# Kernel optimization log

Measured on AMD Instinct MI355X. Metric: run time of the kernel, lower is better.

The kernel has to match this reference:

```python
import jax, jax.numpy as jnp
import numpy as np

S, B, E = 2048, 8, 1024  # seq_len, batch, embed_dim
GAMMA = 0.5              # Kernel(gamma=0.5)


def setup_inputs() -> dict:
    key = jax.random.key(0)
    ks = jax.random.split(key, 4)
    # Weight scale 1/E keeps pairwise squared distances O(1) so the RBF
    # kernel weights are well-conditioned (exp doesn't underflow to all-zeros).
    w_scale = 1.0 / E
    inputs = jax.random.normal(ks[0], (S, B, E), dtype=jnp.float32)
    Wq = jax.random.normal(ks[1], (E, E), dtype=jnp.float32) * w_scale
    Wk = jax.random.normal(ks[2], (E, E), dtype=jnp.float32) * w_scale
    Wv = jax.random.normal(ks[3], (E, E), dtype=jnp.float32) * w_scale
    bq = jnp.zeros((E,), jnp.float32)
    bk = jnp.zeros((E,), jnp.float32)
    bv = jnp.zeros((E,), jnp.float32)
    return {"inputs": inputs, "Wq": Wq, "bq": bq, "Wk": Wk, "bk": bk,
            "Wv": Wv, "bv": bv}


def reference(inputs, Wq, bq, Wk, bk, Wv, bv):
    # QKV projections (nn.Linear: x @ W.T + b)
    q = inputs @ Wq.T + bq  # (S, B, E)
    k = inputs @ Wk.T + bk  # (S, B, E)
    v = inputs @ Wv.T + bv  # (S, B, E)

    # Pairwise RBF kernel sim[t, j, b] = exp(-gamma * ||q[t,b] - k[j,b]||^2)
    # (vectorized replacement of the original O(S^2) python double loop),
    # via ||q||^2 + ||k||^2 - 2 q.k expansion (GEMM-shaped contraction).
    q2 = jnp.sum(q * q, axis=-1)                 # (S, B)
    k2 = jnp.sum(k * k, axis=-1)                 # (S, B)
    qk = jnp.einsum('tbe,jbe->tjb', q, k)        # (S, S, B)
    d2 = q2[:, None, :] + k2[None, :, :] - 2.0 * qk
    d2 = jnp.maximum(d2, 0.0)

    # sim / sim.sum(dim=1) with sim = exp(-gamma*d2) is exactly
    # softmax(-gamma*d2) over axis 1 (the j axis) -- numerically stable form.
    sim = jax.nn.softmax(-GAMMA * d2, axis=1)    # (S, S, B): (t, j, b)

    # Aggregate values: out[t, b, e] = sum_j sim[t, j, b] * v[j, b, e]
    return jnp.einsum('tjb,jbe->tbe', sim, v)    # (S, B, E)
```

## Files before the change

kernel.cpp:

```cpp
#include <hip/hip_runtime.h>
#include <stdint.h>

#define S_LEN 2048
#define BATCH 8
#define EMB   1024
#define GAMMA 0.5f

typedef unsigned short ushort_t;
typedef __attribute__((ext_vector_type(8))) short  short8;
typedef __attribute__((ext_vector_type(8))) unsigned short ushort8;
typedef __attribute__((ext_vector_type(4))) float  floatx4;

__device__ __forceinline__ ushort_t f2bf(float f) {
  uint32_t x = __float_as_uint(f);
  x += 0x7fffu + ((x >> 16) & 1u);
  return (ushort_t)(x >> 16);
}

__device__ __forceinline__ void gl_lds16(const ushort_t* g, ushort_t* l) {
  __builtin_amdgcn_global_load_lds(
      (const __attribute__((address_space(1))) unsigned int*)g,
      (__attribute__((address_space(3))) unsigned int*)l, 16, 0, 0);
}


__device__ __forceinline__ void stage_half(const ushort_t* __restrict__ G,
                                           int ld, int kcol,
                                           ushort_t* lregion, int wave, int lane) {
  const int r4 = lane >> 2;
  const int slot = (lane & 3) ^ ((r4 >> 1) & 3);
  const ushort_t* g = G + (size_t)(wave * 32 + r4) * ld + kcol + slot * 8;
  gl_lds16(g, lregion + wave * 1024);
  gl_lds16(g + (size_t)16 * ld, lregion + wave * 1024 + 512);
}

__device__ __forceinline__ short8 lds_frag(const ushort_t* region, int row, int q) {
  return *(const short8*)(region + row * 32 + (((q ^ (row >> 1)) & 3) << 3));
}

#define MFMA_16(AR, B0, B1, J0, J1)                                            \
  __builtin_amdgcn_s_setprio(1);                                               \
  _Pragma("unroll")                                                            \
  for (int i = 0; i < 8; ++i) {                                                \
    acc[i][J0] = __builtin_amdgcn_mfma_f32_16x16x32_bf16(AR[i], B0, acc[i][J0], 0, 0, 0); \
    acc[i][J1] = __builtin_amdgcn_mfma_f32_16x16x32_bf16(AR[i], B1, acc[i][J1], 0, 0, 0); \
  }                                                                            \
  __builtin_amdgcn_s_setprio(0);

#define INTERVAL_OPEN()                                                        \
  __builtin_amdgcn_s_barrier();                                                \
  asm volatile("s_waitcnt lgkmcnt(0)" ::: "memory");                           \
  __builtin_amdgcn_sched_barrier(0);

__device__ __forceinline__ void gemm8_core(
    const ushort_t* __restrict__ A, const ushort_t* __restrict__ B,
    int lda, int ldb, int K, ushort_t* smem, floatx4 (&acc)[8][4])
{
  const int tid = threadIdx.x;
  const int wave = tid >> 6, lane = tid & 63;
  const int wm = wave >> 2, wn = wave & 3;
  const int lr = lane & 15, q = lane >> 4;
  const int NT = K >> 6;
  const int ra = wm * 128 + lr;
  const int rb = wn * 64 + lr;

  stage_half(A, lda, 0,  smem +     0, wave, lane);
  stage_half(B, ldb, 0,  smem + 16384, wave, lane);
  stage_half(A, lda, 32, smem +  8192, wave, lane);
  stage_half(B, ldb, 32, smem + 24576, wave, lane);
  stage_half(A, lda, 64, smem + 32768, wave, lane);
  stage_half(B, ldb, 64, smem + 49152, wave, lane);
  stage_half(A, lda, 96, smem + 40960, wave, lane);
  asm volatile("s_waitcnt vmcnt(6)" ::: "memory");
  __builtin_amdgcn_s_barrier();
  __builtin_amdgcn_sched_barrier(0);

  short8 ar[8], ar2[8], b0, b1, t0, t1, u0, u1;
#pragma unroll
  for (int i = 0; i < 8; ++i) ar[i] = lds_frag(smem, ra + i * 16, q);
  b0 = lds_frag(smem + 16384, rb,      q);
  b1 = lds_frag(smem + 16384, rb + 16, q);

  for (int kt = 0; kt < NT; ++kt) {
    ushort_t* const cur = smem + (kt & 1) * 32768;
    ushort_t* const nxt = smem + ((kt & 1) ^ 1) * 32768;
    const bool s1 = (kt + 1) < NT, s2 = (kt + 2) < NT;

    INTERVAL_OPEN()
    MFMA_16(ar, b0, b1, 0, 1)
    t0 = lds_frag(cur + 16384, rb + 32, q);
    t1 = lds_frag(cur + 16384, rb + 48, q);
#pragma unroll
    for (int i = 0; i < 4; ++i) ar2[i] = lds_frag(cur + 8192, ra + i * 16, q);
    if (s1) stage_half(B, ldb, (kt + 1) * 64 + 32, nxt + 24576, wave, lane);

    INTERVAL_OPEN()
    MFMA_16(ar, t0, t1, 2, 3)
#pragma unroll
    for (int i = 4; i < 8; ++i) ar2[i] = lds_frag(cur + 8192, ra + i * 16, q);
    u0 = lds_frag(cur + 24576, rb,      q);
    u1 = lds_frag(cur + 24576, rb + 16, q);
    if (s2) stage_half(A, lda, (kt + 2) * 64, cur, wave, lane);

    INTERVAL_OPEN()
    MFMA_16(ar2, u0, u1, 0, 1)
    t0 = lds_frag(cur + 24576, rb + 32, q);
    t1 = lds_frag(cur + 24576, rb + 48, q);
    if (s2) stage_half(B, ldb, (kt + 2) * 64, cur + 16384, wave, lane);
    if (s1) {
      if (s2) { asm volatile("s_waitcnt vmcnt(4)" ::: "memory"); }
      else    { asm volatile("s_waitcnt vmcnt(0)" ::: "memory"); }
    }

    INTERVAL_OPEN()
    MFMA_16(ar2, t0, t1, 2, 3)
    if (s1) {
#pragma unroll
      for (int i = 0; i < 8; ++i) ar[i] = lds_frag(nxt, ra + i * 16, q);
      b0 = lds_frag(nxt + 16384, rb,      q);
      b1 = lds_frag(nxt + 16384, rb + 16, q);
    }
    if (s2) stage_half(A, lda, (kt + 2) * 64 + 32, cur + 8192, wave, lane);
  }
}

__global__ __launch_bounds__(256) void k_quant_x(const float* __restrict__ X,
                                                 ushort_t* __restrict__ Xb) {
  size_t i = ((size_t)blockIdx.x * 256 + threadIdx.x) * 4;
  float4 v = *(const float4*)(X + i);
  *(ushort4*)(Xb + i) = make_ushort4(f2bf(v.x), f2bf(v.y), f2bf(v.z), f2bf(v.w));
}

__global__ __launch_bounds__(256) void k_quant_w(
    const float* __restrict__ Wq, const float* __restrict__ Wk,
    const float* __restrict__ Wv, ushort_t* __restrict__ W) {
  size_t i = ((size_t)blockIdx.x * 256 + threadIdx.x) * 4;
  int row = (int)(i >> 10), col = (int)(i & 1023);
  int sel = row >> 10, sr = row & 1023;
  const float* src = sel == 0 ? Wq : (sel == 1 ? Wk : Wv);
  float4 v = *(const float4*)(src + (size_t)sr * 1024 + col);
  *(ushort4*)(W + i) = make_ushort4(f2bf(v.x), f2bf(v.y), f2bf(v.z), f2bf(v.w));
}

__global__ __launch_bounds__(256) void k_bias_zero(
    const float* __restrict__ bq, const float* __restrict__ bk,
    const float* __restrict__ bv, float* __restrict__ bias,
    float* __restrict__ q2, float* __restrict__ k2, float* __restrict__ rsum) {
  int i = blockIdx.x * 256 + threadIdx.x;
  if (i < 1024)       bias[i] = bq[i];
  else if (i < 2048)  bias[i] = bk[i - 1024];
  else if (i < 3072)  bias[i] = bv[i - 2048];
  if (i < BATCH * S_LEN) { q2[i] = 0.f; k2[i] = 0.f; rsum[i] = 0.f; }
}

__global__ __launch_bounds__(512, 2) void k_gemm_qkv(
    const ushort_t* __restrict__ Xb, const ushort_t* __restrict__ W,
    const float* __restrict__ bias,
    ushort_t* __restrict__ Q, ushort_t* __restrict__ Kp, ushort_t* __restrict__ V,
    float* __restrict__ q2, float* __restrict__ k2) {
  __shared__ __attribute__((aligned(16))) ushort_t smem[65536];
  const int mt = blockIdx.x * 256, nt = blockIdx.y * 256;
  floatx4 acc[8][4];
  const floatx4 z = {0.f, 0.f, 0.f, 0.f};
#pragma unroll
  for (int i = 0; i < 8; ++i)
#pragma unroll
    for (int j = 0; j < 4; ++j) acc[i][j] = z;

  gemm8_core(Xb + (size_t)mt * EMB, W + (size_t)nt * EMB, EMB, EMB, EMB, smem, acc);

  const int lane = threadIdx.x & 63, wave = threadIdx.x >> 6;
  const int wm = wave >> 2, wn = wave & 3;
  const int lr = lane & 15, q = lane >> 4;
  const int which = nt >> 10;
  const int nc0 = nt & 1023;
  ushort_t* dst = which == 0 ? Q : (which == 1 ? Kp : V);
  float* sq = which == 0 ? q2 : k2;
  float bv4[4];
#pragma unroll
  for (int j = 0; j < 4; ++j) bv4[j] = bias[nt + wn * 64 + j * 16 + lr];

#pragma unroll
  for (int i = 0; i < 8; ++i) {
#pragma unroll
    for (int r = 0; r < 4; ++r) {
      const int g = mt + wm * 128 + i * 16 + q * 4 + r;
      const int t = g >> 3, b = g & 7;
      float ss = 0.f;
#pragma unroll
      for (int j = 0; j < 4; ++j) {
        const float val = acc[i][j][r] + bv4[j];
        dst[(size_t)(b * S_LEN + t) * EMB + nc0 + wn * 64 + j * 16 + lr] = f2bf(val);
        ss += val * val;
      }
      if (which < 2) {
        ss += __shfl_xor(ss, 1);
        ss += __shfl_xor(ss, 2);
        ss += __shfl_xor(ss, 4);
        ss += __shfl_xor(ss, 8);
        if (lr == 0) atomicAdd(&sq[b * S_LEN + t], ss);
      }
    }
  }
}

__global__ __launch_bounds__(256) void k_transpose(const ushort_t* __restrict__ V,
                                                   ushort_t* __restrict__ Vt) {
  __shared__ ushort_t tile[64][72];
  const int b = blockIdx.z, j0 = blockIdx.x * 64, e0 = blockIdx.y * 64;
  const ushort_t* src = V + ((size_t)b * S_LEN + j0) * EMB + e0;
  const int tid = threadIdx.x;
#pragma unroll
  for (int rep = 0; rep < 2; ++rep) {
    const int lin = rep * 256 + tid;
    const int j = lin >> 3, e8 = (lin & 7) * 8;
    *(uint4*)&tile[j][e8] = *(const uint4*)(src + (size_t)j * EMB + e8);
  }
  __syncthreads();
  ushort_t* dst = Vt + ((size_t)b * EMB + e0) * S_LEN + j0;
#pragma unroll
  for (int rep = 0; rep < 2; ++rep) {
    const int lin = rep * 256 + tid;
    const int e = lin >> 3, j8 = (lin & 7) * 8;
    ushort8 o;
#pragma unroll
    for (int m = 0; m < 8; ++m) o[m] = tile[j8 + m][e];
    *(ushort8*)(dst + (size_t)e * S_LEN + j8) = o;
  }
}

__global__ __launch_bounds__(512, 2) void k_logits(
    const ushort_t* __restrict__ Q, const ushort_t* __restrict__ Kp,
    const float* __restrict__ q2, const float* __restrict__ k2,
    ushort_t* __restrict__ P, float* __restrict__ rsum) {
  __shared__ __attribute__((aligned(16))) ushort_t smem[65536];
  const int b = blockIdx.z;
  const int mt = blockIdx.x * 256, nt = blockIdx.y * 256;
  floatx4 acc[8][4];
  const floatx4 z = {0.f, 0.f, 0.f, 0.f};
#pragma unroll
  for (int i = 0; i < 8; ++i)
#pragma unroll
    for (int j = 0; j < 4; ++j) acc[i][j] = z;

  gemm8_core(Q + ((size_t)b * S_LEN + mt) * EMB,
             Kp + ((size_t)b * S_LEN + nt) * EMB, EMB, EMB, EMB, smem, acc);

  const int lane = threadIdx.x & 63, wave = threadIdx.x >> 6;
  const int wm = wave >> 2, wn = wave & 3;
  const int lr = lane & 15, q = lane >> 4;
  float k2v[4];
#pragma unroll
  for (int j = 0; j < 4; ++j) k2v[j] = k2[b * S_LEN + nt + wn * 64 + j * 16 + lr];

#pragma unroll
  for (int i = 0; i < 8; ++i) {
#pragma unroll
    for (int r = 0; r < 4; ++r) {
      const int t = mt + wm * 128 + i * 16 + q * 4 + r;
      const float q2v = q2[b * S_LEN + t];
      float ss = 0.f;
#pragma unroll
      for (int j = 0; j < 4; ++j) {
        float d2 = q2v + k2v[j] - 2.f * acc[i][j][r];
        d2 = fmaxf(d2, 0.f);
        const float p = __expf(-GAMMA * d2);
        P[((size_t)b * S_LEN + t) * S_LEN + nt + wn * 64 + j * 16 + lr] = f2bf(p);
        ss += p;
      }
      ss += __shfl_xor(ss, 1);
      ss += __shfl_xor(ss, 2);
      ss += __shfl_xor(ss, 4);
      ss += __shfl_xor(ss, 8);
      if (lr == 0) atomicAdd(&rsum[b * S_LEN + t], ss);
    }
  }
}

__global__ __launch_bounds__(512, 2) void k_out(
    const ushort_t* __restrict__ P, const ushort_t* __restrict__ Vt,
    const float* __restrict__ rsum, float* __restrict__ out) {
  __shared__ __attribute__((aligned(16))) ushort_t smem[65536];
  const int b = blockIdx.z;
  const int mt = blockIdx.x * 256, nt = blockIdx.y * 256;
  floatx4 acc[8][4];
  const floatx4 z = {0.f, 0.f, 0.f, 0.f};
#pragma unroll
  for (int i = 0; i < 8; ++i)
#pragma unroll
    for (int j = 0; j < 4; ++j) acc[i][j] = z;

  gemm8_core(P + ((size_t)b * S_LEN + mt) * S_LEN,
             Vt + ((size_t)b * EMB + nt) * S_LEN, S_LEN, S_LEN, S_LEN, smem, acc);

  const int lane = threadIdx.x & 63, wave = threadIdx.x >> 6;
  const int wm = wave >> 2, wn = wave & 3;
  const int lr = lane & 15, q = lane >> 4;
#pragma unroll
  for (int i = 0; i < 8; ++i) {
#pragma unroll
    for (int r = 0; r < 4; ++r) {
      const int t = mt + wm * 128 + i * 16 + q * 4 + r;
      const float rinv = 1.f / rsum[b * S_LEN + t];
#pragma unroll
      for (int j = 0; j < 4; ++j) {
        const int e = nt + wn * 64 + j * 16 + lr;
        out[((size_t)t * BATCH + b) * EMB + e] = acc[i][j][r] * rinv;
      }
    }
  }
}

extern "C" void kernel_launch(void* const* d_in, const int* in_sizes, int n_in,
                              void* d_out, int out_size, void* d_ws, size_t ws_size,
                              hipStream_t stream) {
  (void)in_sizes; (void)n_in; (void)out_size; (void)ws_size;
  const float* X  = (const float*)d_in[0];
  const float* Wq = (const float*)d_in[1];
  const float* bq = (const float*)d_in[2];
  const float* Wk = (const float*)d_in[3];
  const float* bk = (const float*)d_in[4];
  const float* Wv = (const float*)d_in[5];
  const float* bv = (const float*)d_in[6];
  float* out = (float*)d_out;
  char* ws = (char*)d_ws;

  ushort_t* Q    = (ushort_t*)(ws + 0);
  ushort_t* Kp   = (ushort_t*)(ws + 33554432);
  ushort_t* V    = (ushort_t*)(ws + 67108864);
  ushort_t* Vt   = (ushort_t*)(ws + 100663296);
  ushort_t* P    = (ushort_t*)(ws + 134217728);
  ushort_t* Xb   = (ushort_t*)(ws + 134217728);
  ushort_t* Wqkv = (ushort_t*)(ws + 201326592);
  float*    bias = (float*)(ws + 207618048);
  float*    q2   = (float*)(ws + 207630336);
  float*    k2   = (float*)(ws + 207695872);
  float*    rsum = (float*)(ws + 207761408);

  k_quant_x <<<16384, 256, 0, stream>>>(X, Xb);
  k_quant_w <<<3072, 256, 0, stream>>>(Wq, Wk, Wv, Wqkv);
  k_bias_zero<<<64, 256, 0, stream>>>(bq, bk, bv, bias, q2, k2, rsum);
  k_gemm_qkv<<<dim3(64, 12), 512, 0, stream>>>(Xb, Wqkv, bias, Q, Kp, V, q2, k2);
  k_transpose<<<dim3(32, 16, 8), 256, 0, stream>>>(V, Vt);
  k_logits  <<<dim3(8, 8, 8), 512, 0, stream>>>(Q, Kp, q2, k2, P, rsum);
  k_out     <<<dim3(8, 4, 8), 512, 0, stream>>>(P, Vt, rsum, out);
}
```

Measured before the change: 403.4 us.

## Restructure GEMM main loop into two intervals with batched prefetch

```diff
diff --git a/kernel.cpp b/kernel.cpp
--- a/kernel.cpp
+++ b/kernel.cpp
@@ -39,13 +39,11 @@
 }
 
 #define MFMA_16(AR, B0, B1, J0, J1)                                            \
-  __builtin_amdgcn_s_setprio(1);                                               \
   _Pragma("unroll")                                                            \
   for (int i = 0; i < 8; ++i) {                                                \
     acc[i][J0] = __builtin_amdgcn_mfma_f32_16x16x32_bf16(AR[i], B0, acc[i][J0], 0, 0, 0); \
     acc[i][J1] = __builtin_amdgcn_mfma_f32_16x16x32_bf16(AR[i], B1, acc[i][J1], 0, 0, 0); \
-  }                                                                            \
-  __builtin_amdgcn_s_setprio(0);
+  }
 
 #define INTERVAL_OPEN()                                                        \
   __builtin_amdgcn_s_barrier();                                                \
@@ -70,16 +68,17 @@
   stage_half(B, ldb, 32, smem + 24576, wave, lane);
   stage_half(A, lda, 64, smem + 32768, wave, lane);
   stage_half(B, ldb, 64, smem + 49152, wave, lane);
-  stage_half(A, lda, 96, smem + 40960, wave, lane);
-  asm volatile("s_waitcnt vmcnt(6)" ::: "memory");
+  asm volatile("s_waitcnt vmcnt(4)" ::: "memory");
   __builtin_amdgcn_s_barrier();
   __builtin_amdgcn_sched_barrier(0);
 
-  short8 ar[8], ar2[8], b0, b1, t0, t1, u0, u1;
+  short8 ar[8], ar2[8], b0, b1, t0, t1, u0, u1, v0, v1;
 #pragma unroll
   for (int i = 0; i < 8; ++i) ar[i] = lds_frag(smem, ra + i * 16, q);
   b0 = lds_frag(smem + 16384, rb,      q);
   b1 = lds_frag(smem + 16384, rb + 16, q);
+  t0 = lds_frag(smem + 16384, rb + 32, q);
+  t1 = lds_frag(smem + 16384, rb + 48, q);
 
   for (int kt = 0; kt < NT; ++kt) {
     ushort_t* const cur = smem + (kt & 1) * 32768;
@@ -87,40 +86,41 @@
     const bool s1 = (kt + 1) < NT, s2 = (kt + 2) < NT;
 
     INTERVAL_OPEN()
-    MFMA_16(ar, b0, b1, 0, 1)
-    t0 = lds_frag(cur + 16384, rb + 32, q);
-    t1 = lds_frag(cur + 16384, rb + 48, q);
-#pragma unroll
-    for (int i = 0; i < 4; ++i) ar2[i] = lds_frag(cur + 8192, ra + i * 16, q);
-    if (s1) stage_half(B, ldb, (kt + 1) * 64 + 32, nxt + 24576, wave, lane);
-
-    INTERVAL_OPEN()
-    MFMA_16(ar, t0, t1, 2, 3)
-#pragma unroll
-    for (int i = 4; i < 8; ++i) ar2[i] = lds_frag(cur + 8192, ra + i * 16, q);
+#pragma unroll
+    for (int i = 0; i < 8; ++i) ar2[i] = lds_frag(cur + 8192, ra + i * 16, q);
     u0 = lds_frag(cur + 24576, rb,      q);
     u1 = lds_frag(cur + 24576, rb + 16, q);
-    if (s2) stage_half(A, lda, (kt + 2) * 64, cur, wave, lane);
+    v0 = lds_frag(cur + 24576, rb + 32, q);
+    v1 = lds_frag(cur + 24576, rb + 48, q);
+    if (s1) {
+      stage_half(A, lda, (kt + 1) * 64 + 32, nxt +  8192, wave, lane);
+      stage_half(B, ldb, (kt + 1) * 64 + 32, nxt + 24576, wave, lane);
+    }
+    __builtin_amdgcn_s_setprio(1);
+    MFMA_16(ar, b0, b1, 0, 1)
+    MFMA_16(ar, t0, t1, 2, 3)
+    __builtin_amdgcn_s_setprio(0);
+    if (s1) { asm volatile("s_waitcnt vmcnt(4)" ::: "memory"); }
 
     INTERVAL_OPEN()
-    MFMA_16(ar2, u0, u1, 0, 1)
-    t0 = lds_frag(cur + 24576, rb + 32, q);
-    t1 = lds_frag(cur + 24576, rb + 48, q);
-    if (s2) stage_half(B, ldb, (kt + 2) * 64, cur + 16384, wave, lane);
-    if (s1) {
-      if (s2) { asm volatile("s_waitcnt vmcnt(4)" ::: "memory"); }
-      else    { asm volatile("s_waitcnt vmcnt(0)" ::: "memory"); }
-    }
-
-    INTERVAL_OPEN()
-    MFMA_16(ar2, t0, t1, 2, 3)
     if (s1) {
 #pragma unroll
       for (int i = 0; i < 8; ++i) ar[i] = lds_frag(nxt, ra + i * 16, q);
       b0 = lds_frag(nxt + 16384, rb,      q);
       b1 = lds_frag(nxt + 16384, rb + 16, q);
-    }
-    if (s2) stage_half(A, lda, (kt + 2) * 64 + 32, cur + 8192, wave, lane);
+      t0 = lds_frag(nxt + 16384, rb + 32, q);
+      t1 = lds_frag(nxt + 16384, rb + 48, q);
+    }
+    if (s2) {
+      stage_half(A, lda, (kt + 2) * 64, cur,         wave, lane);
+      stage_half(B, ldb, (kt + 2) * 64, cur + 16384, wave, lane);
+    }
+    __builtin_amdgcn_s_setprio(1);
+    MFMA_16(ar2, u0, u1, 0, 1)
+    MFMA_16(ar2, v0, v1, 2, 3)
+    __builtin_amdgcn_s_setprio(0);
+    if (s2)      { asm volatile("s_waitcnt vmcnt(4)" ::: "memory"); }
+    else if (s1) { asm volatile("s_waitcnt vmcnt(0)" ::: "memory"); }
   }
 }
 
```

New measurement: 403.7 us. About the same (+0.1%).

## Reorder GEMM pipeline phases and remap block indices across XCDs

Applied to the files above, without the earlier changes.

```diff
diff --git a/kernel.cpp b/kernel.cpp
--- a/kernel.cpp
+++ b/kernel.cpp
@@ -24,33 +24,21 @@
 }
 
 
-__device__ __forceinline__ void stage_half(const ushort_t* __restrict__ G,
-                                           int ld, int kcol,
-                                           ushort_t* lregion, int wave, int lane) {
-  const int r4 = lane >> 2;
-  const int slot = (lane & 3) ^ ((r4 >> 1) & 3);
-  const ushort_t* g = G + (size_t)(wave * 32 + r4) * ld + kcol + slot * 8;
-  gl_lds16(g, lregion + wave * 1024);
-  gl_lds16(g + (size_t)16 * ld, lregion + wave * 1024 + 512);
-}
-
 __device__ __forceinline__ short8 lds_frag(const ushort_t* region, int row, int q) {
   return *(const short8*)(region + row * 32 + (((q ^ (row >> 1)) & 3) << 3));
 }
 
 #define MFMA_16(AR, B0, B1, J0, J1)                                            \
-  __builtin_amdgcn_s_setprio(1);                                               \
   _Pragma("unroll")                                                            \
   for (int i = 0; i < 8; ++i) {                                                \
     acc[i][J0] = __builtin_amdgcn_mfma_f32_16x16x32_bf16(AR[i], B0, acc[i][J0], 0, 0, 0); \
     acc[i][J1] = __builtin_amdgcn_mfma_f32_16x16x32_bf16(AR[i], B1, acc[i][J1], 0, 0, 0); \
-  }                                                                            \
-  __builtin_amdgcn_s_setprio(0);
-
-#define INTERVAL_OPEN()                                                        \
+  }
+
+#define PHASE_END()                                                            \
+  asm volatile("s_waitcnt lgkmcnt(0)" ::: "memory");                           \
   __builtin_amdgcn_s_barrier();                                                \
-  asm volatile("s_waitcnt lgkmcnt(0)" ::: "memory");                           \
-  __builtin_amdgcn_sched_barrier(0);
+  asm volatile("" ::: "memory");
 
 __device__ __forceinline__ void gemm8_core(
     const ushort_t* __restrict__ A, const ushort_t* __restrict__ B,
@@ -63,17 +51,31 @@
   const int NT = K >> 6;
   const int ra = wm * 128 + lr;
   const int rb = wn * 64 + lr;
-
-  stage_half(A, lda, 0,  smem +     0, wave, lane);
-  stage_half(B, ldb, 0,  smem + 16384, wave, lane);
-  stage_half(A, lda, 32, smem +  8192, wave, lane);
-  stage_half(B, ldb, 32, smem + 24576, wave, lane);
-  stage_half(A, lda, 64, smem + 32768, wave, lane);
-  stage_half(B, ldb, 64, smem + 49152, wave, lane);
-  stage_half(A, lda, 96, smem + 40960, wave, lane);
+  const int r4 = lane >> 2;
+  const int slot = (lane & 3) ^ ((r4 >> 1) & 3);
+  ushort_t* const lw = smem + wave * 1024;
+
+  const ushort_t* pA0 = A + (size_t)(wave * 32 + r4) * lda + slot * 8;
+  const ushort_t* pA1 = pA0 + (size_t)16 * lda;
+  const ushort_t* pB0 = B + (size_t)(wave * 32 + r4) * ldb + slot * 8;
+  const ushort_t* pB1 = pB0 + (size_t)16 * ldb;
+
+  auto stA = [&](int regionOff, int koff) {
+    gl_lds16(pA0 + koff, lw + regionOff);
+    gl_lds16(pA1 + koff, lw + regionOff + 512);
+  };
+  auto stB = [&](int regionOff, int koff) {
+    gl_lds16(pB0 + koff, lw + regionOff);
+    gl_lds16(pB1 + koff, lw + regionOff + 512);
+  };
+
+  stA(0, 0);      stB(16384, 0);
+  stA(8192, 32);  stB(24576, 32);
+  stA(32768, 64); stB(49152, 64);
+  stA(40960, 96);
   asm volatile("s_waitcnt vmcnt(6)" ::: "memory");
   __builtin_amdgcn_s_barrier();
-  __builtin_amdgcn_sched_barrier(0);
+  asm volatile("" ::: "memory");
 
   short8 ar[8], ar2[8], b0, b1, t0, t1, u0, u1;
 #pragma unroll
@@ -82,45 +84,54 @@
   b1 = lds_frag(smem + 16384, rb + 16, q);
 
   for (int kt = 0; kt < NT; ++kt) {
-    ushort_t* const cur = smem + (kt & 1) * 32768;
-    ushort_t* const nxt = smem + ((kt & 1) ^ 1) * 32768;
+    const int bo = (kt & 1) * 32768;
+    const int bn = bo ^ 32768;
+    ushort_t* const cur = smem + bo;
+    ushort_t* const nxt = smem + bn;
     const bool s1 = (kt + 1) < NT, s2 = (kt + 2) < NT;
-
-    INTERVAL_OPEN()
-    MFMA_16(ar, b0, b1, 0, 1)
+    const int k1 = (kt + 1) << 6, k2 = (kt + 2) << 6;
+
     t0 = lds_frag(cur + 16384, rb + 32, q);
     t1 = lds_frag(cur + 16384, rb + 48, q);
 #pragma unroll
     for (int i = 0; i < 4; ++i) ar2[i] = lds_frag(cur + 8192, ra + i * 16, q);
-    if (s1) stage_half(B, ldb, (kt + 1) * 64 + 32, nxt + 24576, wave, lane);
-
-    INTERVAL_OPEN()
-    MFMA_16(ar, t0, t1, 2, 3)
+    if (s1) stB(bn + 24576, k1 + 32);
+    __builtin_amdgcn_s_setprio(1);
+    MFMA_16(ar, b0, b1, 0, 1)
+    __builtin_amdgcn_s_setprio(0);
+    PHASE_END()
+
 #pragma unroll
     for (int i = 4; i < 8; ++i) ar2[i] = lds_frag(cur + 8192, ra + i * 16, q);
     u0 = lds_frag(cur + 24576, rb,      q);
     u1 = lds_frag(cur + 24576, rb + 16, q);
-    if (s2) stage_half(A, lda, (kt + 2) * 64, cur, wave, lane);
-
-    INTERVAL_OPEN()
-    MFMA_16(ar2, u0, u1, 0, 1)
+    if (s2) stA(bo, k2);
+    __builtin_amdgcn_s_setprio(1);
+    MFMA_16(ar, t0, t1, 2, 3)
+    __builtin_amdgcn_s_setprio(0);
+    PHASE_END()
+
     t0 = lds_frag(cur + 24576, rb + 32, q);
     t1 = lds_frag(cur + 24576, rb + 48, q);
-    if (s2) stage_half(B, ldb, (kt + 2) * 64, cur + 16384, wave, lane);
-    if (s1) {
-      if (s2) { asm volatile("s_waitcnt vmcnt(4)" ::: "memory"); }
-      else    { asm volatile("s_waitcnt vmcnt(0)" ::: "memory"); }
-    }
-
-    INTERVAL_OPEN()
-    MFMA_16(ar2, t0, t1, 2, 3)
+    if (s2) stB(bo + 16384, k2);
+    __builtin_amdgcn_s_setprio(1);
+    MFMA_16(ar2, u0, u1, 0, 1)
+    __builtin_amdgcn_s_setprio(0);
+    if (s2)      { asm volatile("s_waitcnt vmcnt(4)" ::: "memory"); }
+    else if (s1) { asm volatile("s_waitcnt vmcnt(0)" ::: "memory"); }
+    PHASE_END()
+
     if (s1) {
 #pragma unroll
       for (int i = 0; i < 8; ++i) ar[i] = lds_frag(nxt, ra + i * 16, q);
       b0 = lds_frag(nxt + 16384, rb,      q);
       b1 = lds_frag(nxt + 16384, rb + 16, q);
     }
-    if (s2) stage_half(A, lda, (kt + 2) * 64 + 32, cur + 8192, wave, lane);
+    if (s2) stA(bo + 8192, k2 + 32);
+    __builtin_amdgcn_s_setprio(1);
+    MFMA_16(ar2, t0, t1, 2, 3)
+    __builtin_amdgcn_s_setprio(0);
+    PHASE_END()
   }
 }
 
@@ -159,7 +170,10 @@
     ushort_t* __restrict__ Q, ushort_t* __restrict__ Kp, ushort_t* __restrict__ V,
     float* __restrict__ q2, float* __restrict__ k2) {
   __shared__ __attribute__((aligned(16))) ushort_t smem[65536];
-  const int mt = blockIdx.x * 256, nt = blockIdx.y * 256;
+  const int lin = blockIdx.x + (blockIdx.y << 6);
+  const int mt_i = (lin & 7) * 8 + ((lin >> 3) & 7);
+  const int nt_i = lin >> 6;
+  const int mt = mt_i * 256, nt = nt_i * 256;
   floatx4 acc[8][4];
   const floatx4 z = {0.f, 0.f, 0.f, 0.f};
 #pragma unroll
@@ -234,8 +248,10 @@
     const float* __restrict__ q2, const float* __restrict__ k2,
     ushort_t* __restrict__ P, float* __restrict__ rsum) {
   __shared__ __attribute__((aligned(16))) ushort_t smem[65536];
-  const int b = blockIdx.z;
-  const int mt = blockIdx.x * 256, nt = blockIdx.y * 256;
+  const int lin = blockIdx.x + (blockIdx.y << 3) + (blockIdx.z << 6);
+  const int b = lin & 7;
+  const int seq = lin >> 3;
+  const int mt = (seq & 7) * 256, nt = (seq >> 3) * 256;
   floatx4 acc[8][4];
   const floatx4 z = {0.f, 0.f, 0.f, 0.f};
 #pragma unroll
@@ -281,8 +297,10 @@
     const ushort_t* __restrict__ P, const ushort_t* __restrict__ Vt,
     const float* __restrict__ rsum, float* __restrict__ out) {
   __shared__ __attribute__((aligned(16))) ushort_t smem[65536];
-  const int b = blockIdx.z;
-  const int mt = blockIdx.x * 256, nt = blockIdx.y * 256;
+  const int lin = blockIdx.x + (blockIdx.y << 3) + (blockIdx.z << 5);
+  const int b = lin & 7;
+  const int seq = lin >> 3;
+  const int mt = (seq & 7) * 256, nt = (seq >> 3) * 256;
   floatx4 acc[8][4];
   const floatx4 z = {0.f, 0.f, 0.f, 0.f};
 #pragma unroll
```

New measurement: 399.8 us. About the same (-0.9%).
